# Optimization experiments

Measured on AMD Instinct MI355X. Metric: run time of the kernel, lower is better.

Reference implementation:

```python
import jax, jax.numpy as jnp
import numpy as np

B, S, H = 2, 2048, 4096
NH, NKV, HD = 32, 8, 128
THETA = 1000000.0
NEG = jnp.finfo(jnp.float32).min


def setup_inputs() -> dict:
    key = jax.random.key(0)
    ks = jax.random.split(key, 9)
    s = 0.02
    return {
        "hidden_states": jax.random.normal(ks[0], (B, S, H), jnp.float32),
        "position_ids": jnp.tile(jnp.arange(S, dtype=jnp.int32)[None, :], (B, 1)),
        "Wq": jax.random.normal(ks[1], (NH * HD, H), jnp.float32) * s,
        "bq": jax.random.normal(ks[2], (NH * HD,), jnp.float32) * s,
        "Wk": jax.random.normal(ks[3], (NKV * HD, H), jnp.float32) * s,
        "bk": jax.random.normal(ks[4], (NKV * HD,), jnp.float32) * s,
        "Wv": jax.random.normal(ks[5], (NKV * HD, H), jnp.float32) * s,
        "bv": jax.random.normal(ks[6], (NKV * HD,), jnp.float32) * s,
        "Wo": jax.random.normal(ks[7], (H, H), jnp.float32) * s,
        "bo": jax.random.normal(ks[8], (H,), jnp.float32) * s,
    }


def _rotate_half_interleaved(x):
    # y[..., ::2] = -x[..., 1::2]; y[..., 1::2] = x[..., ::2]
    x2 = x.reshape(*x.shape[:-1], -1, 2)
    y = jnp.stack([-x2[..., 1], x2[..., 0]], axis=-1)
    return y.reshape(x.shape)


def reference(hidden_states, position_ids, Wq, bq, Wk, bk, Wv, bv, Wo, bo):
    bsz, q_len, _ = hidden_states.shape
    q = (hidden_states @ Wq.T + bq).reshape(bsz, q_len, NH, HD).transpose(0, 2, 1, 3)
    k = (hidden_states @ Wk.T + bk).reshape(bsz, q_len, NKV, HD).transpose(0, 2, 1, 3)
    v = (hidden_states @ Wv.T + bv).reshape(bsz, q_len, NKV, HD).transpose(0, 2, 1, 3)

    # rotary embedding (interleaved / repeat_interleave variant)
    inv_freq = 1.0 / (THETA ** (jnp.arange(0, HD, 2, dtype=jnp.float32) / HD))
    freqs = position_ids.astype(jnp.float32)[:, :, None] * inv_freq[None, None, :]  # [B,S,HD/2]
    emb = jnp.repeat(freqs, 2, axis=-1)  # [B,S,HD]
    cos = jnp.cos(emb)[:, None, :, :]  # [B,1,S,HD]
    sin = jnp.sin(emb)[:, None, :, :]
    q = q * cos + _rotate_half_interleaved(q) * sin
    k = k * cos + _rotate_half_interleaved(k) * sin

    # GQA: repeat KV heads (repeat_interleave on head axis)
    n_rep = NH // NKV
    k = jnp.repeat(k, n_rep, axis=1)
    v = jnp.repeat(v, n_rep, axis=1)

    scores = jnp.einsum("bhqd,bhkd->bhqk", q, k) / np.sqrt(HD).astype(np.float32)
    causal = jnp.tril(jnp.ones((q_len, q_len), dtype=bool))
    scores = jnp.where(causal[None, None, :, :], scores, NEG)
    attn = jax.nn.softmax(scores.astype(jnp.float32), axis=-1).astype(q.dtype)
    out = jnp.einsum("bhqk,bhkd->bhqd", attn, v)
    out = out.transpose(0, 2, 1, 3).reshape(bsz, q_len, H)
    return out @ Wo.T + bo
```

## Files before the change

### kernel.cpp

```cpp
#include <hip/hip_runtime.h>
#include <stdint.h>

typedef __bf16 bf16x8 __attribute__((ext_vector_type(8)));
typedef float f32x4 __attribute__((ext_vector_type(4)));
typedef float f32x16 __attribute__((ext_vector_type(16)));

#define S_LEN 2048
#define NKVH 8
#define HDIM 128
#define MROWS 4096
#define LDQKV 6144
#define SCALE 0.08838834764831845f
#define C_LOG2 0.1275405707067851f
#define THR_RAW 62.7f

__device__ __forceinline__ unsigned short f2bf(float f) {
  unsigned u = __float_as_uint(f);
  u += 0x7FFFu + ((u >> 16) & 1u);
  return (unsigned short)(u >> 16);
}
__device__ __forceinline__ float bf2f(unsigned short h) {
  return __uint_as_float(((unsigned)h) << 16);
}

__device__ __forceinline__ void gload16(const unsigned short* g, unsigned short* l) {
  __builtin_amdgcn_global_load_lds(
      (__attribute__((address_space(1))) void*)(g),
      (__attribute__((address_space(3))) void*)(l), 16, 0, 0);
}

__global__ void cast_f32_bf16(const float4* __restrict__ in, ushort4* __restrict__ out, int n4) {
  int i = blockIdx.x * 256 + threadIdx.x;
  const int stride = gridDim.x * 256;
  for (; i < n4; i += stride) {
    float4 v = in[i];
    ushort4 o;
    o.x = f2bf(v.x); o.y = f2bf(v.y); o.z = f2bf(v.z); o.w = f2bf(v.w);
    out[i] = o;
  }
}

template <int OUTF>
__global__ __launch_bounds__(512, 2)
void gemm256(const unsigned short* __restrict__ A,
             const unsigned short* __restrict__ Bw,
             const float* __restrict__ bias,
             void* __restrict__ C,
             int ldc, int K) {
  __shared__ unsigned short lds[8][8192];

  const int t = threadIdx.x;
  const int lane = t & 63;
  const int w = t >> 6;
  const int wr = w >> 2, wc = w & 3;
  const int row16 = lane & 15, kgrp = lane >> 4;
  const int m0 = blockIdx.y * 256, n0 = blockIdx.x * 256;

  const int riu = t >> 3;
  const int col = (((t & 7) ^ (riu & 7)) << 3);
  const int rB0 = (riu & 31) + ((riu >> 5) << 6);
  const unsigned short* pA = A + (size_t)(m0 + riu) * K + col;
  const unsigned short* pB = Bw + (size_t)(n0 + rB0) * K + col;

#define STGU(SL, SRC)                                                       \
  {                                                                         \
    gload16((SRC), &lds[SL][t * 8]);                                        \
    gload16((SRC) + (size_t)128 * K, &lds[SL][4096 + t * 8]);               \
  }
#define RDA(SL)                                                             \
  _Pragma("unroll") for (int mi = 0; mi < 4; mi++)                          \
  _Pragma("unroll") for (int ks = 0; ks < 2; ks++)                          \
    afr[mi][ks] = *(const bf16x8*)(&lds[SL][0] + abase + mi * 1024 +        \
                                   ((((ks << 2) + kgrp) ^ sw) << 3));
#define RDB(SL, W)                                                          \
  _Pragma("unroll") for (int nj = 0; nj < 2; nj++)                          \
  _Pragma("unroll") for (int ks = 0; ks < 2; ks++)                          \
    bfr[W][nj][ks] = *(const bf16x8*)(&lds[SL][0] + bbase + nj * 1024 +     \
                                      ((((ks << 2) + kgrp) ^ sw) << 3));
#define MM(MO, NO, W)                                                       \
  __builtin_amdgcn_s_setprio(1);                                            \
  _Pragma("unroll") for (int mi = 0; mi < 4; mi++)                          \
  _Pragma("unroll") for (int nj = 0; nj < 2; nj++)                          \
  _Pragma("unroll") for (int ks = 0; ks < 2; ks++)                          \
    acc[(MO) + mi][(NO) + nj] = __builtin_amdgcn_mfma_f32_16x16x32_bf16(    \
        afr[mi][ks], bfr[W][nj][ks], acc[(MO) + mi][(NO) + nj], 0, 0, 0);   \
  __builtin_amdgcn_s_setprio(0);
#define BAR __builtin_amdgcn_s_barrier()

  const int sw = row16 & 7;
  const int abase = (wr * 64 + row16) * 64;
  const int bbase = (wc * 32 + row16) * 64;

  f32x4 acc[8][4];
#pragma unroll
  for (int i = 0; i < 8; i++)
#pragma unroll
    for (int j = 0; j < 4; j++) acc[i][j] = (f32x4){0.f, 0.f, 0.f, 0.f};

  bf16x8 afr[4][2], bfr[2][2][2];
  const int NT = K >> 6;
  const int NI = NT >> 1;

  STGU(0, pA);
  STGU(1, pB);
  STGU(2, pB + (size_t)32 * K);
  STGU(3, pA + (size_t)64 * K);
  STGU(4, pA + 64);
  STGU(5, pB + 64);
  STGU(6, pB + (size_t)32 * K + 64);
  asm volatile("s_waitcnt vmcnt(6)" ::: "memory");
  BAR;

  for (int I = 0; I < NI; ++I) {
    const size_t k1 = ((size_t)(2 * I + 1)) << 6;
    const size_t k2 = ((size_t)(2 * I + 2)) << 6;
    const size_t k3 = ((size_t)(2 * I + 3)) << 6;
    const bool s2 = (I + 1 < NI);

    RDA(0); RDB(1, 0);
    STGU(7, pA + (size_t)64 * K + k1);
    BAR;
    MM(0, 0, 0);
    BAR;
    RDB(2, 1);
    if (s2) STGU(0, pA + k2);
    BAR;
    MM(0, 2, 1);
    BAR;
    RDA(3);
    if (s2) STGU(1, pB + k2);
    BAR;
    MM(4, 2, 1);
    BAR;
    if (s2) {
      STGU(2, pB + (size_t)32 * K + k2);
      asm volatile("s_waitcnt vmcnt(6)" ::: "memory");
    } else {
      asm volatile("s_waitcnt vmcnt(0)" ::: "memory");
    }
    BAR;
    MM(4, 0, 0);
    BAR;
    RDA(4); RDB(5, 0);
    if (s2) STGU(3, pA + (size_t)64 * K + k2);
    BAR;
    MM(0, 0, 0);
    BAR;
    RDB(6, 1);
    if (s2) STGU(4, pA + k3);
    BAR;
    MM(0, 2, 1);
    BAR;
    RDA(7);
    if (s2) STGU(5, pB + k3);
    BAR;
    MM(4, 2, 1);
    BAR;
    if (s2) {
      STGU(6, pB + (size_t)32 * K + k3);
      asm volatile("s_waitcnt vmcnt(6)" ::: "memory");
    } else {
      asm volatile("s_waitcnt vmcnt(0)" ::: "memory");
    }
    BAR;
    MM(4, 0, 0);
    BAR;
  }
#undef STGU
#undef RDA
#undef RDB
#undef MM
#undef BAR

#pragma unroll
  for (int MI = 0; MI < 8; MI++) {
#pragma unroll
    for (int NJ = 0; NJ < 4; NJ++) {
      const int gr = m0 + wr * 128 + MI * 16 + kgrp * 4;
      const int gc = n0 + wc * 64 + NJ * 16 + row16;
      const float bv = bias[gc];
#pragma unroll
      for (int jj = 0; jj < 4; jj++) {
        float v = acc[MI][NJ][jj] + bv;
        if (OUTF) ((float*)C)[(size_t)(gr + jj) * ldc + gc] = v;
        else ((unsigned short*)C)[(size_t)(gr + jj) * ldc + gc] = f2bf(v);
      }
    }
  }
}

template <int OUTF>
__global__ __launch_bounds__(512, 2)
void gemm128(const unsigned short* __restrict__ A,
             const unsigned short* __restrict__ Bw,
             const float* __restrict__ bias,
             void* __restrict__ C,
             int ldc, int K) {
  __shared__ unsigned short lds[3 * 24576];

  const int t = threadIdx.x;
  const int lane = t & 63;
  const int w = t >> 6;
  const int wr = w >> 2, wc = w & 3;
  const int row16 = lane & 15, kgrp = lane >> 4;
  const int m0 = blockIdx.y * 128, n0 = blockIdx.x * 256;

  const int riu = t >> 3;
  const int col = (((t & 7) ^ (riu & 7)) << 3);
  const unsigned short* pA = A + (size_t)(m0 + riu) * K + col;
  const unsigned short* pB = Bw + (size_t)(n0 + riu) * K + col;

#define STG6(bo_, kk_)                                                      \
  {                                                                         \
    gload16(pA + (kk_), &lds[(bo_) + t * 8]);                               \
    gload16(pA + (size_t)64 * K + (kk_), &lds[(bo_) + 4096 + t * 8]);       \
    gload16(pB + (kk_), &lds[(bo_) + 8192 + t * 8]);                        \
    gload16(pB + (size_t)64 * K + (kk_), &lds[(bo_) + 12288 + t * 8]);      \
    gload16(pB + (size_t)128 * K + (kk_), &lds[(bo_) + 16384 + t * 8]);     \
    gload16(pB + (size_t)192 * K + (kk_), &lds[(bo_) + 20480 + t * 8]);     \
  }

  const int sw = row16 & 7;
  const int abase = (wr * 64 + row16) * 64;
  const int bbase = 8192 + (wc * 64 + row16) * 64;

  f32x4 acc[4][4];
#pragma unroll
  for (int i = 0; i < 4; i++)
#pragma unroll
    for (int j = 0; j < 4; j++) acc[i][j] = (f32x4){0.f, 0.f, 0.f, 0.f};

  bf16x8 afr[4][2], bfr[4][2];
  const int NT = K >> 6;

  STG6(0, 0);
  STG6(24576, 64);

  int rbc = 0;
  int rbs = 2;
  for (int T = 0; T < NT; ++T) {
    if (T < NT - 1) { asm volatile("s_waitcnt vmcnt(6)\n\ts_barrier" ::: "memory"); }
    else            { asm volatile("s_waitcnt vmcnt(0)\n\ts_barrier" ::: "memory"); }
    if (T + 2 < NT) STG6(rbs * 24576, (size_t)(T + 2) << 6);
    const unsigned short* Lc = &lds[rbc * 24576];

#pragma unroll
    for (int mi = 0; mi < 4; mi++)
#pragma unroll
      for (int ks = 0; ks < 2; ks++)
        afr[mi][ks] = *(const bf16x8*)(Lc + abase + mi * 1024 + ((((ks << 2) + kgrp) ^ sw) << 3));
#pragma unroll
    for (int nj = 0; nj < 4; nj++)
#pragma unroll
      for (int ks = 0; ks < 2; ks++)
        bfr[nj][ks] = *(const bf16x8*)(Lc + bbase + nj * 1024 + ((((ks << 2) + kgrp) ^ sw) << 3));

    __builtin_amdgcn_s_setprio(1);
#pragma unroll
    for (int mi = 0; mi < 4; mi++)
#pragma unroll
      for (int nj = 0; nj < 4; nj++)
#pragma unroll
        for (int ks = 0; ks < 2; ks++)
          acc[mi][nj] = __builtin_amdgcn_mfma_f32_16x16x32_bf16(afr[mi][ks], bfr[nj][ks], acc[mi][nj], 0, 0, 0);
    __builtin_amdgcn_s_setprio(0);

    rbc++; if (rbc == 3) rbc = 0;
    rbs++; if (rbs == 3) rbs = 0;
  }
#undef STG6

#pragma unroll
  for (int MI = 0; MI < 4; MI++) {
#pragma unroll
    for (int NJ = 0; NJ < 4; NJ++) {
      const int gr = m0 + wr * 64 + MI * 16 + kgrp * 4;
      const int gc = n0 + wc * 64 + NJ * 16 + row16;
      const float bv = bias[gc];
#pragma unroll
      for (int jj = 0; jj < 4; jj++) {
        float v = acc[MI][NJ][jj] + bv;
        if (OUTF) ((float*)C)[(size_t)(gr + jj) * ldc + gc] = v;
        else ((unsigned short*)C)[(size_t)(gr + jj) * ldc + gc] = f2bf(v);
      }
    }
  }
}

__global__ void rope_kernel(unsigned short* __restrict__ X,
                            const int* __restrict__ pos_ids,
                            int ncols, int ld) {
  const int perrow = ncols >> 3;
  int idx = blockIdx.x * 256 + threadIdx.x;
  const int row = idx / perrow;
  const int c0 = (idx - row * perrow) << 3;
  const float pos = (float)pos_ids[row];
  unsigned short* p = X + (size_t)row * ld + c0;
  uint4 v = *(uint4*)p;
  unsigned short* e = (unsigned short*)&v;
  const int p0 = (c0 & 127) >> 1;
#pragma unroll
  for (int q = 0; q < 4; ++q) {
    const float inv = exp2f(-(float)(p0 + q) * (19.931568569324174f / 64.f));
    const float fr = pos * inv;
    float sn, cs;
    __sincosf(fr, &sn, &cs);
    const float xe = bf2f(e[2 * q]);
    const float xo = bf2f(e[2 * q + 1]);
    e[2 * q]     = f2bf(xe * cs - xo * sn);
    e[2 * q + 1] = f2bf(xo * cs + xe * sn);
  }
  *(uint4*)p = v;
}

__global__ void transpose_v(const unsigned short* __restrict__ V, int ldv,
                            unsigned short* __restrict__ Vt) {
  __shared__ unsigned short tile[32][40];
  const int t = threadIdx.x;
  const int n0 = blockIdx.x * 32;
  const int m0 = blockIdx.y * 32;
  const int r = t >> 3;
  const int c = (t & 7) << 2;
  const unsigned short* src = V + (size_t)(m0 + r) * ldv + n0 + c;
  ushort4 d = *(const ushort4*)src;
  tile[r][c] = d.x; tile[r][c + 1] = d.y; tile[r][c + 2] = d.z; tile[r][c + 3] = d.w;
  __syncthreads();
  const int b = m0 >> 11;
  unsigned short* dst = Vt + (size_t)(b * 1024 + n0 + r) * 2048 + (m0 & 2047) + c;
  ushort4 o;
  o.x = tile[c][r]; o.y = tile[c + 1][r]; o.z = tile[c + 2][r]; o.w = tile[c + 3][r];
  *(ushort4*)dst = o;
}

__global__ __launch_bounds__(256, 2)
void attn_kernel3(const unsigned short* __restrict__ QKV,
                  const unsigned short* __restrict__ Vt,
                  unsigned short* __restrict__ O) {
  __shared__ unsigned short sK[2 * 2 * 64 * 64];
  __shared__ unsigned short sV[2 * 128 * 64];

  const int t = threadIdx.x;
  const int lane = t & 63;
  const int w = t >> 6;
  const int l31 = lane & 31;
  const int hi = lane >> 5;
  const int bid = blockIdx.x;
  const int g = bid >> 6, bh = bid & 63;
  const int qt = (g < 8) ? (15 - g) : (g - 8);
  const int b = bh >> 5, h = bh & 31;
  const int kh = h >> 2;
  const int q0 = qt << 7;
  const int qw = q0 + w * 32;
  const int qg = qw + l31;

  const int ntiles = (q0 + 128) >> 6;
  const int myTiles = (qw + 95) >> 6;

  const int kr5 = t >> 3;
  const int ksw2 = ((t & 7) ^ (kr5 & 7)) << 3;
  const int vrow0 = t >> 3;
  const int vslot = t & 7;
  const unsigned short* Kp = QKV + (size_t)(b * S_LEN) * LDQKV + 4096 + kh * HDIM;
  const unsigned short* Vp = Vt + (size_t)(b * 1024 + kh * HDIM) * 2048;
  const int vsw = (vslot ^ (vrow0 & 7)) << 3;
  const unsigned short* KpA = Kp + (size_t)kr5 * LDQKV + ksw2;
  const unsigned short* VpA = Vp + (size_t)vrow0 * 2048 + vsw;

#define STAGE(bufi, kv0m)                                                      \
  {                                                                            \
    _Pragma("unroll")                                                          \
    for (int p = 0; p < 4; p++)                                                \
      gload16(KpA + (size_t)((kv0m) + ((p & 1) << 5)) * LDQKV + ((p >> 1) << 6), \
              &sK[(bufi) * 8192 + p * 2048 + t * 8]);                          \
    _Pragma("unroll")                                                          \
    for (int p = 0; p < 4; p++)                                                \
      gload16(VpA + (kv0m) + p * 65536, &sV[(bufi) * 8192 + p * 2048 + t * 8]); \
  }

  bf16x8 qf[8];
  {
    const unsigned short* qb = QKV + (size_t)(b * S_LEN + qw + l31) * LDQKV + h * HDIM + hi * 8;
#pragma unroll
    for (int kd = 0; kd < 8; kd++) qf[kd] = *(const bf16x8*)(qb + kd * 16);
  }

  f32x16 o[4];
#pragma unroll
  for (int nt = 0; nt < 4; nt++)
#pragma unroll
    for (int r = 0; r < 16; r++) o[nt][r] = 0.f;
  float m = -1e30f, lsum = 0.f;

  const int rw7 = (l31 & 7) << 4;
  const int kswz = (hi << 4) ^ rw7;
  const int kbase = l31 << 6;
  const int vbase = l31 * 64;

  STAGE(0, 0);
  int buf = 0;
  for (int it = 0; it < ntiles; ++it) {
    if (it + 1 < ntiles) {
      STAGE(buf ^ 1, (it + 1) << 6);
      asm volatile("s_waitcnt vmcnt(8)" ::: "memory");
    } else {
      asm volatile("s_waitcnt vmcnt(0)" ::: "memory");
    }
    __builtin_amdgcn_s_barrier();

    if (it < myTiles) {
      const unsigned short* sKc = sK + buf * 8192;
      const unsigned short* sVc = sV + buf * 8192;
      const int kv0 = it << 6;

      f32x16 st[2];
#pragma unroll
      for (int r = 0; r < 16; r++) { st[0][r] = 0.f; st[1][r] = 0.f; }
      __builtin_amdgcn_s_setprio(1);
#pragma unroll
      for (int kd = 0; kd < 8; kd++) {
        const int koff = ((kd >> 2) << 12) + ((((kd & 3) << 5) ^ kswz) >> 1);
        bf16x8 k0 = *(const bf16x8*)(sKc + koff + kbase);
        bf16x8 k1 = *(const bf16x8*)(sKc + koff + kbase + 2048);
        st[0] = __builtin_amdgcn_mfma_f32_32x32x16_bf16(k0, qf[kd], st[0], 0, 0, 0);
        st[1] = __builtin_amdgcn_mfma_f32_32x32x16_bf16(k1, qf[kd], st[1], 0, 0, 0);
      }
      __builtin_amdgcn_s_setprio(0);

      if (it == myTiles - 1) {
#pragma unroll
        for (int s2 = 0; s2 < 2; s2++)
#pragma unroll
          for (int r = 0; r < 16; r++) {
            const int kvg = kv0 + s2 * 32 + (r & 3) + 8 * (r >> 2) + 4 * hi;
            if (kvg > qg) st[s2][r] = -1e30f;
          }
      }

      float mx[8];
#pragma unroll
      for (int r = 0; r < 8; r++)
        mx[r] = fmaxf(fmaxf(st[0][r], st[0][r + 8]), fmaxf(st[1][r], st[1][r + 8]));
#pragma unroll
      for (int d = 4; d >= 1; d >>= 1)
#pragma unroll
        for (int r = 0; r < d; r++) mx[r] = fmaxf(mx[r], mx[r + d]);
      float tmax = fmaxf(mx[0], __shfl_xor(mx[0], 32));

      if (!__all(tmax <= m + THR_RAW)) {
        const float mnew = fmaxf(m, tmax);
        const float corr = exp2f((m - mnew) * C_LOG2);
        lsum *= corr;
#pragma unroll
        for (int r = 0; r < 16; r++) {
          const int src = (r & 3) + 8 * (r >> 2) + 4 * hi;
          const float cr = __shfl(corr, src);
#pragma unroll
          for (int nt = 0; nt < 4; nt++) o[nt][r] *= cr;
        }
        m = mnew;
      }
      const float mC = m * C_LOG2;

#pragma unroll
      for (int s2 = 0; s2 < 2; s2++)
#pragma unroll
        for (int r = 0; r < 16; r++) st[s2][r] = exp2f(fmaf(st[s2][r], C_LOG2, -mC));
      float sm[8];
#pragma unroll
      for (int r = 0; r < 8; r++)
        sm[r] = (st[0][r] + st[0][r + 8]) + (st[1][r] + st[1][r + 8]);
#pragma unroll
      for (int d = 4; d >= 1; d >>= 1)
#pragma unroll
        for (int r = 0; r < d; r++) sm[r] += sm[r + d];
      float tsum = sm[0] + __shfl_xor(sm[0], 32);
      lsum += tsum;

      bf16x8 pa[4];
#pragma unroll
      for (int s2 = 0; s2 < 2; s2++) {
        unsigned pw[8];
#pragma unroll
        for (int i = 0; i < 8; i++)
          asm("v_cvt_pk_bf16_f32 %0, %1, %2" : "=v"(pw[i]) : "v"(st[s2][2 * i]), "v"(st[s2][2 * i + 1]));
        const unsigned x0 = (unsigned)__shfl_xor((int)pw[0], 32);
        const unsigned x1 = (unsigned)__shfl_xor((int)pw[1], 32);
        const unsigned x2 = (unsigned)__shfl_xor((int)pw[2], 32);
        const unsigned x3 = (unsigned)__shfl_xor((int)pw[3], 32);
        const unsigned x4 = (unsigned)__shfl_xor((int)pw[4], 32);
        const unsigned x5 = (unsigned)__shfl_xor((int)pw[5], 32);
        const unsigned x6 = (unsigned)__shfl_xor((int)pw[6], 32);
        const unsigned x7 = (unsigned)__shfl_xor((int)pw[7], 32);
        union { unsigned u[4]; bf16x8 v; } u0, u1;
        u0.u[0] = hi ? x2 : pw[0];
        u0.u[1] = hi ? x3 : pw[1];
        u0.u[2] = hi ? pw[2] : x0;
        u0.u[3] = hi ? pw[3] : x1;
        u1.u[0] = hi ? x6 : pw[4];
        u1.u[1] = hi ? x7 : pw[5];
        u1.u[2] = hi ? pw[6] : x4;
        u1.u[3] = hi ? pw[7] : x5;
        pa[2 * s2] = u0.v; pa[2 * s2 + 1] = u1.v;
      }

      __builtin_amdgcn_s_setprio(1);
#pragma unroll
      for (int nt = 0; nt < 4; nt++) {
        const unsigned short* vr = sVc + vbase + nt * 2048;
#pragma unroll
        for (int ks = 0; ks < 4; ks++) {
          bf16x8 vb = *(const bf16x8*)(vr + (((ks << 5) ^ kswz) >> 1));
          o[nt] = __builtin_amdgcn_mfma_f32_32x32x16_bf16(pa[ks], vb, o[nt], 0, 0, 0);
        }
      }
      __builtin_amdgcn_s_setprio(0);
    }

    __builtin_amdgcn_s_barrier();
    buf ^= 1;
  }

  const float linv = 1.0f / lsum;
#pragma unroll
  for (int r = 0; r < 16; r++) {
    const int qr = (r & 3) + 8 * (r >> 2) + 4 * hi;
    const float lr = __shfl(linv, qr);
    unsigned short* orow = O + (size_t)(b * S_LEN + qw + qr) * 4096 + h * HDIM + l31;
#pragma unroll
    for (int nt = 0; nt < 4; nt++) orow[nt * 32] = f2bf(o[nt][r] * lr);
  }
#undef STAGE
}

extern "C" void kernel_launch(void* const* d_in, const int* in_sizes, int n_in,
                              void* d_out, int out_size, void* d_ws, size_t ws_size,
                              hipStream_t stream) {
  const float* hs = (const float*)d_in[0];
  const int*  pos = (const int*)d_in[1];
  const float* Wq = (const float*)d_in[2];
  const float* bq = (const float*)d_in[3];
  const float* Wk = (const float*)d_in[4];
  const float* bk = (const float*)d_in[5];
  const float* Wv = (const float*)d_in[6];
  const float* bv = (const float*)d_in[7];
  const float* Wo = (const float*)d_in[8];
  const float* bo = (const float*)d_in[9];
  float* out = (float*)d_out;

  char* ws = (char*)d_ws;
  unsigned short* hbf  = (unsigned short*)(ws);
  unsigned short* Wbuf = (unsigned short*)(ws + 33554432);
  unsigned short* QKV  = (unsigned short*)(ws + 83886080);
  unsigned short* Vtb  = (unsigned short*)(ws + 134217728);
  float*          biasb= (float*)(ws + 142606336);

  cast_f32_bf16<<<2048, 256, 0, stream>>>((const float4*)hs, (ushort4*)hbf, 4194304);
  cast_f32_bf16<<<2048, 256, 0, stream>>>((const float4*)Wq, (ushort4*)Wbuf, 4194304);
  cast_f32_bf16<<<1024, 256, 0, stream>>>((const float4*)Wk, (ushort4*)(Wbuf + 16777216), 1048576);
  cast_f32_bf16<<<1024, 256, 0, stream>>>((const float4*)Wv, (ushort4*)(Wbuf + 20971520), 1048576);
  hipMemcpyAsync(biasb, bq, 4096 * 4, hipMemcpyDeviceToDevice, stream);
  hipMemcpyAsync(biasb + 4096, bk, 1024 * 4, hipMemcpyDeviceToDevice, stream);
  hipMemcpyAsync(biasb + 5120, bv, 1024 * 4, hipMemcpyDeviceToDevice, stream);

  gemm256<0><<<dim3(16, 16), 512, 0, stream>>>(hbf, Wbuf, biasb, QKV, LDQKV, 4096);
  gemm128<0><<<dim3(8, 32), 512, 0, stream>>>(hbf, Wbuf + 16777216, biasb + 4096, QKV + 4096, LDQKV, 4096);

  cast_f32_bf16<<<2048, 256, 0, stream>>>((const float4*)Wo, (ushort4*)Wbuf, 4194304);

  rope_kernel<<<8192, 256, 0, stream>>>(QKV, pos, 4096, LDQKV);
  rope_kernel<<<2048, 256, 0, stream>>>(QKV + 4096, pos, 1024, LDQKV);

  transpose_v<<<dim3(32, 128), 256, 0, stream>>>(QKV + 5120, LDQKV, Vtb);

  attn_kernel3<<<dim3(1024), 256, 0, stream>>>(QKV, Vtb, hbf);

  gemm256<1><<<dim3(16, 16), 512, 0, stream>>>(hbf, Wbuf, bo, out, 4096, 4096);
}
```

Measured before the change: 524.7 us.

## Fuse RoPE into QKV GEMM epilogues, merge input casts, halve attention shuffles

Applies the rotary embedding directly in the QKV projection GEMM epilogues, using a lane shuffle to fetch the paired element, and removes the two standalone RoPE kernels. This avoids an extra read-modify-write pass over Q and K. The four f32->bf16 casts are merged into one launch, and the P-matrix repack in attention now needs four cross-half shuffles instead of eight. In exchange, the epilogue does per-element sincos and pos loads, and RoPE is now applied to fp32 values before bf16 rounding.

Result: faster. 507.0 us (-3.4%).

```diff
diff --git a/kernel.cpp b/kernel.cpp
--- a/kernel.cpp
+++ b/kernel.cpp
@@ -13,6 +13,7 @@
 #define SCALE 0.08838834764831845f
 #define C_LOG2 0.1275405707067851f
 #define THR_RAW 62.7f
+#define ROPE_L2 0.31143075889569023f
 
 __device__ __forceinline__ unsigned short f2bf(float f) {
   unsigned u = __float_as_uint(f);
@@ -27,6 +28,26 @@
   __builtin_amdgcn_global_load_lds(
       (__attribute__((address_space(1))) void*)(g),
       (__attribute__((address_space(3))) void*)(l), 16, 0, 0);
+}
+
+__global__ void cast4(const float4* __restrict__ s0, const float4* __restrict__ s1,
+                      const float4* __restrict__ s2, const float4* __restrict__ s3,
+                      ushort4* __restrict__ d0, ushort4* __restrict__ d1,
+                      ushort4* __restrict__ d2, ushort4* __restrict__ d3) {
+  const int b = blockIdx.x;
+  const float4* s; ushort4* d; int lb;
+  if (b < 1024)      { s = s0; d = d0; lb = b; }
+  else if (b < 2048) { s = s1; d = d1; lb = b - 1024; }
+  else if (b < 2304) { s = s2; d = d2; lb = b - 2048; }
+  else               { s = s3; d = d3; lb = b - 2304; }
+  int base = lb * 4096 + threadIdx.x;
+#pragma unroll
+  for (int i = 0; i < 16; i++) {
+    float4 v = s[base + i * 256];
+    ushort4 o;
+    o.x = f2bf(v.x); o.y = f2bf(v.y); o.z = f2bf(v.z); o.w = f2bf(v.w);
+    d[base + i * 256] = o;
+  }
 }
 
 __global__ void cast_f32_bf16(const float4* __restrict__ in, ushort4* __restrict__ out, int n4) {
@@ -40,12 +61,13 @@
   }
 }
 
-template <int OUTF>
+template <int OUTF, int ROPE>
 __global__ __launch_bounds__(512, 2)
 void gemm256(const unsigned short* __restrict__ A,
              const unsigned short* __restrict__ Bw,
              const float* __restrict__ bias,
              void* __restrict__ C,
+             const int* __restrict__ pos,
              int ldc, int K) {
   __shared__ unsigned short lds[8][8192];
 
@@ -179,22 +201,37 @@
       const int gr = m0 + wr * 128 + MI * 16 + kgrp * 4;
       const int gc = n0 + wc * 64 + NJ * 16 + row16;
       const float bv = bias[gc];
-#pragma unroll
-      for (int jj = 0; jj < 4; jj++) {
-        float v = acc[MI][NJ][jj] + bv;
-        if (OUTF) ((float*)C)[(size_t)(gr + jj) * ldc + gc] = v;
-        else ((unsigned short*)C)[(size_t)(gr + jj) * ldc + gc] = f2bf(v);
+      if (ROPE) {
+        const int hf = (gc & 127) >> 1;
+        const float inv = exp2f(-(float)hf * ROPE_L2);
+#pragma unroll
+        for (int jj = 0; jj < 4; jj++) {
+          float v = acc[MI][NJ][jj] + bv;
+          float px = __shfl_xor(v, 1);
+          float sn, cs;
+          __sincosf((float)pos[gr + jj] * inv, &sn, &cs);
+          float ov = (gc & 1) ? fmaf(v, cs, px * sn) : fmaf(v, cs, -px * sn);
+          ((unsigned short*)C)[(size_t)(gr + jj) * ldc + gc] = f2bf(ov);
+        }
+      } else {
+#pragma unroll
+        for (int jj = 0; jj < 4; jj++) {
+          float v = acc[MI][NJ][jj] + bv;
+          if (OUTF) ((float*)C)[(size_t)(gr + jj) * ldc + gc] = v;
+          else ((unsigned short*)C)[(size_t)(gr + jj) * ldc + gc] = f2bf(v);
+        }
       }
     }
   }
 }
 
-template <int OUTF>
+template <int OUTF, int ROPE>
 __global__ __launch_bounds__(512, 2)
 void gemm128(const unsigned short* __restrict__ A,
              const unsigned short* __restrict__ Bw,
              const float* __restrict__ bias,
              void* __restrict__ C,
+             const int* __restrict__ pos,
              int ldc, int K) {
   __shared__ unsigned short lds[3 * 24576];
 
@@ -277,40 +314,28 @@
       const int gr = m0 + wr * 64 + MI * 16 + kgrp * 4;
       const int gc = n0 + wc * 64 + NJ * 16 + row16;
       const float bv = bias[gc];
-#pragma unroll
-      for (int jj = 0; jj < 4; jj++) {
-        float v = acc[MI][NJ][jj] + bv;
-        if (OUTF) ((float*)C)[(size_t)(gr + jj) * ldc + gc] = v;
-        else ((unsigned short*)C)[(size_t)(gr + jj) * ldc + gc] = f2bf(v);
+      if (ROPE && gc < 1024) {
+        const int hf = (gc & 127) >> 1;
+        const float inv = exp2f(-(float)hf * ROPE_L2);
+#pragma unroll
+        for (int jj = 0; jj < 4; jj++) {
+          float v = acc[MI][NJ][jj] + bv;
+          float px = __shfl_xor(v, 1);
+          float sn, cs;
+          __sincosf((float)pos[gr + jj] * inv, &sn, &cs);
+          float ov = (gc & 1) ? fmaf(v, cs, px * sn) : fmaf(v, cs, -px * sn);
+          ((unsigned short*)C)[(size_t)(gr + jj) * ldc + gc] = f2bf(ov);
+        }
+      } else {
+#pragma unroll
+        for (int jj = 0; jj < 4; jj++) {
+          float v = acc[MI][NJ][jj] + bv;
+          if (OUTF) ((float*)C)[(size_t)(gr + jj) * ldc + gc] = v;
+          else ((unsigned short*)C)[(size_t)(gr + jj) * ldc + gc] = f2bf(v);
+        }
       }
     }
   }
-}
-
-__global__ void rope_kernel(unsigned short* __restrict__ X,
-                            const int* __restrict__ pos_ids,
-                            int ncols, int ld) {
-  const int perrow = ncols >> 3;
-  int idx = blockIdx.x * 256 + threadIdx.x;
-  const int row = idx / perrow;
-  const int c0 = (idx - row * perrow) << 3;
-  const float pos = (float)pos_ids[row];
-  unsigned short* p = X + (size_t)row * ld + c0;
-  uint4 v = *(uint4*)p;
-  unsigned short* e = (unsigned short*)&v;
-  const int p0 = (c0 & 127) >> 1;
-#pragma unroll
-  for (int q = 0; q < 4; ++q) {
-    const float inv = exp2f(-(float)(p0 + q) * (19.931568569324174f / 64.f));
-    const float fr = pos * inv;
-    float sn, cs;
-    __sincosf(fr, &sn, &cs);
-    const float xe = bf2f(e[2 * q]);
-    const float xo = bf2f(e[2 * q + 1]);
-    e[2 * q]     = f2bf(xe * cs - xo * sn);
-    e[2 * q + 1] = f2bf(xo * cs + xe * sn);
-  }
-  *(uint4*)p = v;
 }
 
 __global__ void transpose_v(const unsigned short* __restrict__ V, int ldv,
@@ -483,23 +508,23 @@
 #pragma unroll
         for (int i = 0; i < 8; i++)
           asm("v_cvt_pk_bf16_f32 %0, %1, %2" : "=v"(pw[i]) : "v"(st[s2][2 * i]), "v"(st[s2][2 * i + 1]));
-        const unsigned x0 = (unsigned)__shfl_xor((int)pw[0], 32);
-        const unsigned x1 = (unsigned)__shfl_xor((int)pw[1], 32);
-        const unsigned x2 = (unsigned)__shfl_xor((int)pw[2], 32);
-        const unsigned x3 = (unsigned)__shfl_xor((int)pw[3], 32);
-        const unsigned x4 = (unsigned)__shfl_xor((int)pw[4], 32);
-        const unsigned x5 = (unsigned)__shfl_xor((int)pw[5], 32);
-        const unsigned x6 = (unsigned)__shfl_xor((int)pw[6], 32);
-        const unsigned x7 = (unsigned)__shfl_xor((int)pw[7], 32);
+        const unsigned y0 = hi ? pw[0] : pw[2];
+        const unsigned y1 = hi ? pw[1] : pw[3];
+        const unsigned y2 = hi ? pw[4] : pw[6];
+        const unsigned y3 = hi ? pw[5] : pw[7];
+        const unsigned x0 = (unsigned)__shfl_xor((int)y0, 32);
+        const unsigned x1 = (unsigned)__shfl_xor((int)y1, 32);
+        const unsigned x2 = (unsigned)__shfl_xor((int)y2, 32);
+        const unsigned x3 = (unsigned)__shfl_xor((int)y3, 32);
         union { unsigned u[4]; bf16x8 v; } u0, u1;
-        u0.u[0] = hi ? x2 : pw[0];
-        u0.u[1] = hi ? x3 : pw[1];
+        u0.u[0] = hi ? x0 : pw[0];
+        u0.u[1] = hi ? x1 : pw[1];
         u0.u[2] = hi ? pw[2] : x0;
         u0.u[3] = hi ? pw[3] : x1;
-        u1.u[0] = hi ? x6 : pw[4];
-        u1.u[1] = hi ? x7 : pw[5];
-        u1.u[2] = hi ? pw[6] : x4;
-        u1.u[3] = hi ? pw[7] : x5;
+        u1.u[0] = hi ? x2 : pw[4];
+        u1.u[1] = hi ? x3 : pw[5];
+        u1.u[2] = hi ? pw[6] : x2;
+        u1.u[3] = hi ? pw[7] : x3;
         pa[2 * s2] = u0.v; pa[2 * s2 + 1] = u1.v;
       }
 
@@ -554,25 +579,21 @@
   unsigned short* Vtb  = (unsigned short*)(ws + 134217728);
   float*          biasb= (float*)(ws + 142606336);
 
-  cast_f32_bf16<<<2048, 256, 0, stream>>>((const float4*)hs, (ushort4*)hbf, 4194304);
-  cast_f32_bf16<<<2048, 256, 0, stream>>>((const float4*)Wq, (ushort4*)Wbuf, 4194304);
-  cast_f32_bf16<<<1024, 256, 0, stream>>>((const float4*)Wk, (ushort4*)(Wbuf + 16777216), 1048576);
-  cast_f32_bf16<<<1024, 256, 0, stream>>>((const float4*)Wv, (ushort4*)(Wbuf + 20971520), 1048576);
+  cast4<<<2560, 256, 0, stream>>>(
+      (const float4*)hs, (const float4*)Wq, (const float4*)Wk, (const float4*)Wv,
+      (ushort4*)hbf, (ushort4*)Wbuf, (ushort4*)(Wbuf + 16777216), (ushort4*)(Wbuf + 20971520));
   hipMemcpyAsync(biasb, bq, 4096 * 4, hipMemcpyDeviceToDevice, stream);
   hipMemcpyAsync(biasb + 4096, bk, 1024 * 4, hipMemcpyDeviceToDevice, stream);
   hipMemcpyAsync(biasb + 5120, bv, 1024 * 4, hipMemcpyDeviceToDevice, stream);
 
-  gemm256<0><<<dim3(16, 16), 512, 0, stream>>>(hbf, Wbuf, biasb, QKV, LDQKV, 4096);
-  gemm128<0><<<dim3(8, 32), 512, 0, stream>>>(hbf, Wbuf + 16777216, biasb + 4096, QKV + 4096, LDQKV, 4096);
+  gemm256<0, 1><<<dim3(16, 16), 512, 0, stream>>>(hbf, Wbuf, biasb, QKV, pos, LDQKV, 4096);
+  gemm128<0, 1><<<dim3(8, 32), 512, 0, stream>>>(hbf, Wbuf + 16777216, biasb + 4096, QKV + 4096, pos, LDQKV, 4096);
 
   cast_f32_bf16<<<2048, 256, 0, stream>>>((const float4*)Wo, (ushort4*)Wbuf, 4194304);
 
-  rope_kernel<<<8192, 256, 0, stream>>>(QKV, pos, 4096, LDQKV);
-  rope_kernel<<<2048, 256, 0, stream>>>(QKV + 4096, pos, 1024, LDQKV);
-
   transpose_v<<<dim3(32, 128), 256, 0, stream>>>(QKV + 5120, LDQKV, Vtb);
 
   attn_kernel3<<<dim3(1024), 256, 0, stream>>>(QKV, Vtb, hbf);
 
-  gemm256<1><<<dim3(16, 16), 512, 0, stream>>>(hbf, Wbuf, bo, out, 4096, 4096);
-}
+  gemm256<1, 0><<<dim3(16, 16), 512, 0, stream>>>(hbf, Wbuf, bo, out, nullptr, 4096, 4096);
+}
```
